# Optimization experiments

Measured on AMD Instinct MI355X. Metric: run time of the kernel, lower is better.

The kernel has to match this reference:

```python
import jax, jax.numpy as jnp
import numpy as np

MARGIN = 0.2  # init margin


def setup_inputs() -> dict:
    key = jax.random.key(0)
    k1, k2, k3, k4 = jax.random.split(key, 4)
    B, Li_raw, Ls_raw, D = 128, 65, 67, 1024
    im_set = jax.random.normal(k1, (B, Li_raw, D), dtype=jnp.float32)
    s_seq = jax.random.normal(k2, (B, Ls_raw, D), dtype=jnp.float32)
    # raw lengths; forward uses im_len-1 and s_len-3, keep them well in range
    im_len = jax.random.randint(k3, (B,), 10, Li_raw + 1)
    s_len = jax.random.randint(k4, (B,), 10, Ls_raw + 1)
    return {"im_set": im_set, "s_seq": s_seq, "im_len": im_len, "s_len": s_len}


def reference(im_set, s_seq, im_len, s_len):
    # slice off CLS-like tokens, as in the torch module
    im = im_set[:, 1:, :]        # [Bi, Li, D]
    s = s_seq[:, 1:-2, :]        # [Bs, Ls, D]
    im_l = im_len - 1
    s_l = s_len - 3
    Bi, Li, D = im.shape
    Bs, Ls, _ = s.shape

    # 4D alignment: all image-batch x sentence-batch token-pair dot products
    align = jnp.einsum('bid,tjd->btij', im, s)  # [Bi, Bs, Li, Ls]

    # length masks (True = padded position), matching the torch loops
    im_mask = jnp.arange(Li)[None, :] >= im_l[:, None]  # [Bi, Li]
    s_mask = jnp.arange(Ls)[None, :] >= s_l[:, None]    # [Bs, Ls]
    mask = im_mask[:, None, :, None] | s_mask[None, :, None, :]
    align = jnp.where(mask, 0.0, align)

    # aggregation 'MrSw': max over image regions, sum over words
    aggr = align.max(axis=2).sum(axis=2)  # [Bi, Bs]

    # contrastive hinge loss with max violation
    diag = jnp.diag(aggr)[:, None]  # [B, 1]
    eye = jnp.eye(Bi, dtype=bool)
    cost_s = jnp.where(eye, 0.0, jnp.maximum(MARGIN + aggr - diag, 0.0))
    cost_im = jnp.where(eye, 0.0, jnp.maximum(MARGIN + aggr - diag.T, 0.0))
    loss = cost_s.max(axis=1).sum() + cost_im.max(axis=0).sum()
    return loss
```

## Files before the change

### kernel.cpp

```cpp
#include <hip/hip_runtime.h>

typedef __attribute__((ext_vector_type(4))) int   i32x4;
typedef __attribute__((ext_vector_type(8))) int   i32x8;
typedef __attribute__((ext_vector_type(16))) float f32x16;

__device__ __forceinline__ unsigned enc4(float v) {
    unsigned s = (__float_as_uint(v) >> 31) << 3;
    float a = fabsf(v);
    unsigned c = a < 0.25f ? 0u : a < 0.75f ? 1u : a < 1.25f ? 2u : a < 1.75f ? 3u
               : a < 2.5f  ? 4u : a < 3.5f  ? 5u : a < 5.0f  ? 6u : 7u;
    return s | c;
}

__global__ void conv_kernel(const float* __restrict__ im, const int* __restrict__ iml,
                            const float* __restrict__ ss, const int* __restrict__ sl,
                            unsigned* __restrict__ Ad, unsigned* __restrict__ Bd)
{
    int bid = blockIdx.x;
    const float* src; const int* len; unsigned* dst; int rawL, adj;
    if (bid < 4096) { src = im; len = iml; dst = Ad; rawL = 65; adj = -1; }
    else { bid -= 4096; src = ss; len = sl; dst = Bd; rawL = 67; adj = -3; }
    int t = threadIdx.x;
    int m = bid * 2 + (t >> 7);
    int c = (t & 127) * 8;
    int b = m >> 6;
    int i = m & 63;
    int lim = len[b] + adj;
    float4 v0 = make_float4(0.f, 0.f, 0.f, 0.f), v1 = v0;
    if (i < lim) {
        const float* p = src + ((size_t)(b * rawL + 1 + i) << 10) + c;
        v0 = *(const float4*)p;
        v1 = *(const float4*)(p + 4);
    }
    unsigned w = enc4(v0.x) | (enc4(v0.y) << 4) | (enc4(v0.z) << 8)  | (enc4(v0.w) << 12)
               | (enc4(v1.x) << 16) | (enc4(v1.y) << 20) | (enc4(v1.z) << 24) | (enc4(v1.w) << 28);
    dst[(m >> 8) * 32768 + (c >> 6) * 2048 + ((c >> 5) & 1) * 1024
        + (m & 255) * 4 + ((c >> 3) & 3)] = w;
}

__device__ __forceinline__ void gload_lds16(const void* g, void* l) {
    __builtin_amdgcn_global_load_lds((const __attribute__((address_space(1))) void*)g,
                                     (__attribute__((address_space(3))) void*)l,
                                     16, 0, 0);
}

__device__ __forceinline__ i32x8 dup4(i32x4 a) {
    return __builtin_shufflevector(a, a, 0, 1, 2, 3, 0, 1, 2, 3);
}

__global__ void __launch_bounds__(512) gemm_aggr_kernel(const unsigned char* __restrict__ A,
                                                        const unsigned char* __restrict__ B,
                                                        float* __restrict__ aggr)
{
    __shared__ __align__(16) char As[4][8192];
    __shared__ __align__(16) char Bs[4][8192];

    const int tid  = threadIdx.x;
    const int lane = tid & 63;
    const int wid  = tid >> 6;
    const int wr   = wid >> 2;
    const int wc   = wid & 3;
    const int tm   = blockIdx.y;
    const int tn   = blockIdx.x;

    const int r31 = lane & 31;
    const int g2  = lane >> 5;

    const unsigned char* gA_t = A + (size_t)tm * 131072 + tid * 16;
    const unsigned char* gB_t = B + (size_t)tn * 131072 + tid * 16;

#define STAGE_A(kt) gload_lds16(gA_t + (kt) * 8192, As[(kt) & 3] + tid * 16)
#define STAGE_B(kt) gload_lds16(gB_t + (kt) * 8192, Bs[(kt) & 3] + tid * 16)

    f32x16 acc[4][2];
#pragma unroll
    for (int mi = 0; mi < 4; ++mi)
#pragma unroll
        for (int ni = 0; ni < 2; ++ni)
#pragma unroll
            for (int r = 0; r < 16; ++r)
                acc[mi][ni][r] = 0.f;

    const int aOff = g2 * 4096 + (wr * 128 + r31) * 16;
    const int bOff = g2 * 4096 + (wc * 64 + r31) * 16;

    i32x4 fa0[4], fb0[2], fa1[4], fb1[2];

    STAGE_A(0); STAGE_B(0);
    STAGE_A(1); STAGE_B(1);
    STAGE_A(2); STAGE_B(2);
    asm volatile("s_waitcnt vmcnt(2)" ::: "memory");
    __builtin_amdgcn_s_barrier();
    __builtin_amdgcn_sched_barrier(0);
    {
        const char* A0 = As[0]; const char* B0 = Bs[0];
#pragma unroll
        for (int mi = 0; mi < 4; ++mi) fa0[mi] = *(const i32x4*)(A0 + aOff + mi * 512);
#pragma unroll
        for (int ni = 0; ni < 2; ++ni) fb0[ni] = *(const i32x4*)(B0 + bOff + ni * 512);
    }

#define MFMA8(CA, CB)                                                       \
    __builtin_amdgcn_s_setprio(1);                                          \
    acc[0][0] = __builtin_amdgcn_mfma_scale_f32_32x32x64_f8f6f4(            \
        dup4(CA[0]), dup4(CB[0]), acc[0][0], 4, 4, 0, 127, 0, 127);         \
    acc[0][1] = __builtin_amdgcn_mfma_scale_f32_32x32x64_f8f6f4(            \
        dup4(CA[0]), dup4(CB[1]), acc[0][1], 4, 4, 0, 127, 0, 127);         \
    acc[1][0] = __builtin_amdgcn_mfma_scale_f32_32x32x64_f8f6f4(            \
        dup4(CA[1]), dup4(CB[0]), acc[1][0], 4, 4, 0, 127, 0, 127);         \
    acc[1][1] = __builtin_amdgcn_mfma_scale_f32_32x32x64_f8f6f4(            \
        dup4(CA[1]), dup4(CB[1]), acc[1][1], 4, 4, 0, 127, 0, 127);         \
    acc[2][0] = __builtin_amdgcn_mfma_scale_f32_32x32x64_f8f6f4(            \
        dup4(CA[2]), dup4(CB[0]), acc[2][0], 4, 4, 0, 127, 0, 127);         \
    acc[2][1] = __builtin_amdgcn_mfma_scale_f32_32x32x64_f8f6f4(            \
        dup4(CA[2]), dup4(CB[1]), acc[2][1], 4, 4, 0, 127, 0, 127);         \
    acc[3][0] = __builtin_amdgcn_mfma_scale_f32_32x32x64_f8f6f4(            \
        dup4(CA[3]), dup4(CB[0]), acc[3][0], 4, 4, 0, 127, 0, 127);         \
    acc[3][1] = __builtin_amdgcn_mfma_scale_f32_32x32x64_f8f6f4(            \
        dup4(CA[3]), dup4(CB[1]), acc[3][1], 4, 4, 0, 127, 0, 127);         \
    __builtin_amdgcn_s_setprio(0);

#define BODY(KT, CA, CB, NA, NB)                                            \
  {                                                                         \
    if ((KT) + 3 <= 15) { STAGE_A((KT) + 3); STAGE_B((KT) + 3); }           \
    if ((KT) < 15) {                                                        \
        const char* An = As[((KT) + 1) & 3];                                \
        const char* Bn = Bs[((KT) + 1) & 3];                                \
        NA[0] = *(const i32x4*)(An + aOff);                                 \
        NA[1] = *(const i32x4*)(An + aOff + 512);                           \
        NA[2] = *(const i32x4*)(An + aOff + 1024);                          \
        NA[3] = *(const i32x4*)(An + aOff + 1536);                          \
        NB[0] = *(const i32x4*)(Bn + bOff);                                 \
        NB[1] = *(const i32x4*)(Bn + bOff + 512);                           \
    }                                                                       \
    MFMA8(CA, CB)                                                           \
    if ((KT) < 15) {                                                        \
        if ((KT) <= 12) { asm volatile("s_waitcnt vmcnt(2)" ::: "memory"); }\
        else            { asm volatile("s_waitcnt vmcnt(0)" ::: "memory"); }\
        __builtin_amdgcn_s_barrier();                                       \
        __builtin_amdgcn_sched_barrier(0);                                  \
    }                                                                       \
  }

    for (int kt2 = 0; kt2 < 8; ++kt2) {
        BODY(kt2 * 2,     fa0, fb0, fa1, fb1);
        BODY(kt2 * 2 + 1, fa1, fb1, fa0, fb0);
    }
#undef STAGE_A
#undef STAGE_B
#undef MFMA8
#undef BODY

#pragma unroll
    for (int h = 0; h < 2; ++h) {
        float cm[2];
#pragma unroll
        for (int ni = 0; ni < 2; ++ni) {
            float m = acc[h * 2][ni][0];
#pragma unroll
            for (int dm = 0; dm < 2; ++dm)
#pragma unroll
                for (int r = 0; r < 16; ++r)
                    m = fmaxf(m, acc[h * 2 + dm][ni][r]);
            m = fmaxf(m, __shfl_xor(m, 32));
            cm[ni] = m;
        }
        float s = cm[0] + cm[1];
        s += __shfl_xor(s, 1);
        s += __shfl_xor(s, 2);
        s += __shfl_xor(s, 4);
        s += __shfl_xor(s, 8);
        s += __shfl_xor(s, 16);
        if (lane == 0) {
            int b = tm * 4 + wr * 2 + h;
            int t = tn * 4 + wc;
            aggr[b * 128 + t] = s;
        }
    }
}

__global__ void loss_stage1(const float* __restrict__ aggr, float* __restrict__ red)
{
    const int x = blockIdx.x;
    const int y = threadIdx.x;
    const float diag = aggr[x * 129];
    float ms = 0.f, mi = 0.f;
    if (y != x) {
        ms = fmaxf(0.2f + aggr[x * 128 + y] - diag, 0.f);
        mi = fmaxf(0.2f + aggr[y * 128 + x] - diag, 0.f);
    }
#pragma unroll
    for (int o = 32; o; o >>= 1) {
        ms = fmaxf(ms, __shfl_xor(ms, o));
        mi = fmaxf(mi, __shfl_xor(mi, o));
    }
    __shared__ float sm[2], si[2];
    if ((y & 63) == 0) { sm[y >> 6] = ms; si[y >> 6] = mi; }
    __syncthreads();
    if (y == 0) red[x] = fmaxf(sm[0], sm[1]) + fmaxf(si[0], si[1]);
}

__global__ void loss_stage2(const float* __restrict__ red, float* __restrict__ out)
{
    float v = red[threadIdx.x];
#pragma unroll
    for (int o = 32; o; o >>= 1) v += __shfl_xor(v, o);
    __shared__ float s[2];
    if ((threadIdx.x & 63) == 0) s[threadIdx.x >> 6] = v;
    __syncthreads();
    if (threadIdx.x == 0) *out = s[0] + s[1];
}

extern "C" void kernel_launch(void* const* d_in, const int* in_sizes, int n_in,
                              void* d_out, int out_size, void* d_ws, size_t ws_size,
                              hipStream_t stream)
{
    const float* im_set = (const float*)d_in[0];
    const float* s_seq  = (const float*)d_in[1];
    const int*   im_len = (const int*)d_in[2];
    const int*   s_len  = (const int*)d_in[3];
    float* out = (float*)d_out;

    unsigned char* Abf = (unsigned char*)d_ws;
    unsigned char* Bbf = (unsigned char*)d_ws + (4u << 20);
    float*         agg = (float*)((char*)d_ws + (8u << 20));
    float*         red = (float*)((char*)d_ws + (8u << 20) + 65536);

    conv_kernel<<<8192, 256, 0, stream>>>(im_set, im_len, s_seq, s_len,
                                          (unsigned*)Abf, (unsigned*)Bbf);

    gemm_aggr_kernel<<<dim3(32, 32), 512, 0, stream>>>(Abf, Bbf, agg);

    loss_stage1<<<128, 128, 0, stream>>>(agg, red);
    loss_stage2<<<1, 128, 0, stream>>>(red, out);
}
```

Baseline: 56.04 us.

## Restage FP4 GEMM pipeline into 3 double-k-tile stages with fewer barriers

```diff
diff --git a/kernel.cpp b/kernel.cpp
--- a/kernel.cpp
+++ b/kernel.cpp
@@ -52,8 +52,8 @@
                                                         const unsigned char* __restrict__ B,
                                                         float* __restrict__ aggr)
 {
-    __shared__ __align__(16) char As[4][8192];
-    __shared__ __align__(16) char Bs[4][8192];
+    __shared__ __align__(16) char As[3][16384];
+    __shared__ __align__(16) char Bs[3][16384];
 
     const int tid  = threadIdx.x;
     const int lane = tid & 63;
@@ -69,8 +69,11 @@
     const unsigned char* gA_t = A + (size_t)tm * 131072 + tid * 16;
     const unsigned char* gB_t = B + (size_t)tn * 131072 + tid * 16;
 
-#define STAGE_A(kt) gload_lds16(gA_t + (kt) * 8192, As[(kt) & 3] + tid * 16)
-#define STAGE_B(kt) gload_lds16(gB_t + (kt) * 8192, Bs[(kt) & 3] + tid * 16)
+#define STAGE(j)                                                              \
+    gload_lds16(gA_t + (2*(j))   * 8192, As[(j) % 3]        + tid * 16);      \
+    gload_lds16(gA_t + (2*(j)+1) * 8192, As[(j) % 3] + 8192 + tid * 16);      \
+    gload_lds16(gB_t + (2*(j))   * 8192, Bs[(j) % 3]        + tid * 16);      \
+    gload_lds16(gB_t + (2*(j)+1) * 8192, Bs[(j) % 3] + 8192 + tid * 16);
 
     f32x16 acc[4][2];
 #pragma unroll
@@ -84,21 +87,22 @@
     const int aOff = g2 * 4096 + (wr * 128 + r31) * 16;
     const int bOff = g2 * 4096 + (wc * 64 + r31) * 16;
 
-    i32x4 fa0[4], fb0[2], fa1[4], fb1[2];
-
-    STAGE_A(0); STAGE_B(0);
-    STAGE_A(1); STAGE_B(1);
-    STAGE_A(2); STAGE_B(2);
-    asm volatile("s_waitcnt vmcnt(2)" ::: "memory");
+    i32x4 faE[4], fbE[2], faO[4], fbO[2];
+
+#define READF(FA, FB, Ab, Bb)                                               \
+    FA[0] = *(const i32x4*)((Ab) + aOff);                                   \
+    FA[1] = *(const i32x4*)((Ab) + aOff + 512);                             \
+    FA[2] = *(const i32x4*)((Ab) + aOff + 1024);                            \
+    FA[3] = *(const i32x4*)((Ab) + aOff + 1536);                            \
+    FB[0] = *(const i32x4*)((Bb) + bOff);                                   \
+    FB[1] = *(const i32x4*)((Bb) + bOff + 512);
+
+    STAGE(0)
+    STAGE(1)
+    asm volatile("s_waitcnt vmcnt(4)" ::: "memory");
     __builtin_amdgcn_s_barrier();
     __builtin_amdgcn_sched_barrier(0);
-    {
-        const char* A0 = As[0]; const char* B0 = Bs[0];
-#pragma unroll
-        for (int mi = 0; mi < 4; ++mi) fa0[mi] = *(const i32x4*)(A0 + aOff + mi * 512);
-#pragma unroll
-        for (int ni = 0; ni < 2; ++ni) fb0[ni] = *(const i32x4*)(B0 + bOff + ni * 512);
-    }
+    READF(faE, fbE, As[0], Bs[0])
 
 #define MFMA8(CA, CB)                                                       \
     __builtin_amdgcn_s_setprio(1);                                          \
@@ -120,34 +124,23 @@
         dup4(CA[3]), dup4(CB[1]), acc[3][1], 4, 4, 0, 127, 0, 127);         \
     __builtin_amdgcn_s_setprio(0);
 
-#define BODY(KT, CA, CB, NA, NB)                                            \
+#define BODY(J)                                                             \
   {                                                                         \
-    if ((KT) + 3 <= 15) { STAGE_A((KT) + 3); STAGE_B((KT) + 3); }           \
-    if ((KT) < 15) {                                                        \
-        const char* An = As[((KT) + 1) & 3];                                \
-        const char* Bn = Bs[((KT) + 1) & 3];                                \
-        NA[0] = *(const i32x4*)(An + aOff);                                 \
-        NA[1] = *(const i32x4*)(An + aOff + 512);                           \
-        NA[2] = *(const i32x4*)(An + aOff + 1024);                          \
-        NA[3] = *(const i32x4*)(An + aOff + 1536);                          \
-        NB[0] = *(const i32x4*)(Bn + bOff);                                 \
-        NB[1] = *(const i32x4*)(Bn + bOff + 512);                           \
+    asm volatile("s_waitcnt vmcnt(0)" ::: "memory");                        \
+    __builtin_amdgcn_s_barrier();                                           \
+    __builtin_amdgcn_sched_barrier(0);                                      \
+    if ((J) + 2 <= 7) { STAGE((J) + 2) }                                    \
+    READF(faO, fbO, As[(J) % 3] + 8192, Bs[(J) % 3] + 8192)    \
+    MFMA8(faE, fbE)                                            \
+    if ((J) < 7) {                                                          \
+        READF(faE, fbE, As[((J) + 1) % 3], Bs[((J) + 1) % 3])     \
     }                                                                       \
-    MFMA8(CA, CB)                                                           \
-    if ((KT) < 15) {                                                        \
-        if ((KT) <= 12) { asm volatile("s_waitcnt vmcnt(2)" ::: "memory"); }\
-        else            { asm volatile("s_waitcnt vmcnt(0)" ::: "memory"); }\
-        __builtin_amdgcn_s_barrier();                                       \
-        __builtin_amdgcn_sched_barrier(0);                                  \
-    }                                                                       \
+    MFMA8(faO, fbO)                                            \
   }
 
-    for (int kt2 = 0; kt2 < 8; ++kt2) {
-        BODY(kt2 * 2,     fa0, fb0, fa1, fb1);
-        BODY(kt2 * 2 + 1, fa1, fb1, fa0, fb0);
-    }
-#undef STAGE_A
-#undef STAGE_B
+    BODY(0) BODY(1) BODY(2) BODY(3) BODY(4) BODY(5) BODY(6) BODY(7)
+#undef STAGE
+#undef READF
 #undef MFMA8
 #undef BODY
 
```

Result: faster. 53.04 us (-5.3%).
